# Optimization experiments

Measured on AMD Instinct MI355X. Metric: run time of the kernel, lower is better.

The kernel has to match this reference:

```python
import jax, jax.numpy as jnp
import numpy as np

WIN = 8          # window_size
DIM = 96         # embedding dim
HEADS = 3        # num_heads
N = WIN * WIN    # tokens per window
B_ = 8192        # total windows (2 images * 64*64 windows)
NUM_WIN = 4096   # windows per image (mask leading dim)


def _relative_position_index():
    # Same construction as the torch module (meshgrid default 'ij').
    ch = np.arange(WIN)
    coords = np.stack(np.meshgrid(ch, ch, indexing="ij"))          # [2, W, W]
    flat = coords.reshape(2, -1)                                     # [2, N]
    rel = flat[:, :, None] - flat[:, None, :]                        # [2, N, N]
    rel = rel.transpose(1, 2, 0).astype(np.int32)                    # [N, N, 2]
    rel[:, :, 0] += WIN - 1
    rel[:, :, 1] += WIN - 1
    rel[:, :, 0] *= 2 * WIN - 1
    return rel.sum(-1)                                               # [N, N] int32


def setup_inputs() -> dict:
    key = jax.random.key(0)
    ks = jax.random.split(key, 8)
    x = jax.random.normal(ks[0], (B_, N, DIM), dtype=jnp.float32)
    mask = jax.random.normal(ks[1], (NUM_WIN, N, N), dtype=jnp.float32)
    s = 0.02
    qkv_w = jax.random.normal(ks[2], (3 * DIM, DIM), dtype=jnp.float32) * s
    qkv_b = jax.random.normal(ks[3], (3 * DIM,), dtype=jnp.float32) * s
    proj_w = jax.random.normal(ks[4], (DIM, DIM), dtype=jnp.float32) * s
    proj_b = jax.random.normal(ks[5], (DIM,), dtype=jnp.float32) * s
    n_bias = (2 * WIN - 1) * (2 * WIN - 1)  # 225
    bias_table = jax.random.normal(ks[6], (n_bias, HEADS), dtype=jnp.float32) * s
    rel_idx = jnp.asarray(_relative_position_index())  # [N, N] int32
    return {"x": x, "mask": mask, "qkv_w": qkv_w, "qkv_b": qkv_b,
            "proj_w": proj_w, "proj_b": proj_b, "bias_table": bias_table,
            "rel_idx": rel_idx}


def reference(x, mask, qkv_w, qkv_b, proj_w, proj_b, bias_table, rel_idx):
    Bw, n, C = x.shape
    hd = C // HEADS
    scale = hd ** (-0.5)
    qkv = (x @ qkv_w.T + qkv_b).reshape(Bw, n, 3, HEADS, hd)
    qkv = jnp.transpose(qkv, (2, 0, 3, 1, 4))
    q, k, v = qkv[0], qkv[1], qkv[2]
    attn = jnp.einsum("bhqd,bhkd->bhqk", q * scale, k)              # [Bw, H, n, n]
    # relative position bias gather: [n, n, H] -> [H, n, n]
    bias = bias_table[rel_idx.reshape(-1)].reshape(n, n, HEADS)
    attn = attn + jnp.transpose(bias, (2, 0, 1))[None]
    # shift mask: broadcast over (batch, heads)
    nw = mask.shape[0]
    attn = attn.reshape(Bw // nw, nw, HEADS, n, n) + mask[None, :, None]
    attn = attn.reshape(Bw, HEADS, n, n)
    attn = jax.nn.softmax(attn, axis=-1)
    out = jnp.einsum("bhqk,bhkd->bhqd", attn, v)                    # [Bw, H, n, hd]
    out = jnp.transpose(out, (0, 2, 1, 3)).reshape(Bw, n, C)
    return out @ proj_w.T + proj_b
```

## Files before the change

### kernel.cpp

```cpp
#include <hip/hip_runtime.h>

typedef __attribute__((ext_vector_type(8))) short short8v;
typedef __attribute__((ext_vector_type(4))) float f32x4;

#define INVLN2 1.4426950408889634f

__device__ __forceinline__ ushort f2bf(float f) {
  union { float f; unsigned int u; } c; c.f = f;
  return (ushort)((c.u + 0x7FFFu + ((c.u >> 16) & 1u)) >> 16);
}

__device__ __forceinline__ unsigned cvtpk(float a, float b) {
  unsigned r;
  asm("v_cvt_pk_bf16_f32 %0, %1, %2" : "=v"(r) : "v"(a), "v"(b));
  return r;
}

__device__ __forceinline__ float exp2w(float x) {
#if __has_builtin(__builtin_amdgcn_exp2f)
  return __builtin_amdgcn_exp2f(x);
#else
  return __expf(x * 0.6931471805599453f);
#endif
}

__device__ __forceinline__ short8v bits8(unsigned a, unsigned b, unsigned c, unsigned d) {
  union { unsigned u[4]; short8v s; } cv;
  cv.u[0] = a; cv.u[1] = b; cv.u[2] = c; cv.u[3] = d;
  return cv.s;
}

__global__ __launch_bounds__(256) void setup_k(
    const float* __restrict__ qkv_w, const float* __restrict__ proj_w,
    const float* __restrict__ bias_table, const int* __restrict__ rel_idx,
    const float* __restrict__ qkv_b,
    ushort* __restrict__ qkv_wb, ushort* __restrict__ proj_wb,
    float* __restrict__ bias_comb, float* __restrict__ qkv_bs) {
  const float qs = 0.17677669529663687f * INVLN2;
  int idx = blockIdx.x * 256 + threadIdx.x;
  if (idx < 27648) {
    qkv_wb[idx] = f2bf(qkv_w[idx] * (idx < 9216 ? qs : 1.0f));
  } else if (idx < 36864) {
    int i = idx - 27648;
    int cw = i / 96, j = i % 96;
    int h = j >> 5, kk = j & 31;
    int g = kk >> 3, b = (kk & 4) >> 2, d = kk & 3;
    int src = h * 32 + 16 * b + 4 * g + d;
    proj_wb[i] = f2bf(proj_w[cw * 96 + src]);
  } else if (idx < 49152) {
    int i = idx - 36864;
    int h = i / 4096, rc = i % 4096;
    bias_comb[i] = bias_table[rel_idx[rc] * 3 + h] * INVLN2;
  } else if (idx < 49440) {
    int i = idx - 49152;
    qkv_bs[i] = qkv_b[i] * (i < 96 ? qs : 1.0f);
  }
}

__global__ __launch_bounds__(256, 2) void winattn(
    const float* __restrict__ x, const float* __restrict__ mask,
    const ushort* __restrict__ qkv_wb, const ushort* __restrict__ proj_wb,
    const float* __restrict__ bias_comb, const float* __restrict__ qkv_bs,
    const float* __restrict__ proj_b, float* __restrict__ out) {
  __shared__ ushort klds[2][64][104];
  __shared__ ushort vts[2][96][64];
  __shared__ ushort wq[29952];

  const int bb = blockIdx.x;
  const int t = threadIdx.x;
  const int w = t >> 6;
  const int lane = t & 63;
  const int l15 = lane & 15;
  const int g = lane >> 4;
  const int qrow = w * 16 + l15;

  float4 xr4[2][3][2];
  #pragma unroll
  for (int u = 0; u < 2; ++u) {
    const float* xr = x + ((size_t)(bb + u * 4096) * 64 + qrow) * 96 + g * 8;
    #pragma unroll
    for (int ks3 = 0; ks3 < 3; ++ks3) {
      xr4[u][ks3][0] = *reinterpret_cast<const float4*>(xr + ks3 * 32);
      xr4[u][ks3][1] = *reinterpret_cast<const float4*>(xr + ks3 * 32 + 4);
    }
  }
  const float* mrow = mask + (size_t)bb * 4096 + qrow * 64;
  float4 mk4[4];
  #pragma unroll
  for (int tj = 0; tj < 4; ++tj)
    mk4[tj] = *reinterpret_cast<const float4*>(mrow + tj * 16 + g * 4);

  #pragma unroll
  for (int i = 0; i < 14; ++i) {
    const int c = i * 256 + t;
    if (i < 13 || t < 128) {
      const int row = c / 12, cc = c % 12;
      short8v wv = *reinterpret_cast<const short8v*>(qkv_wb + row * 96 + cc * 8);
      *reinterpret_cast<short8v*>(&wq[row * 104 + cc * 8]) = wv;
    }
  }
  __syncthreads();

  short8v xa[2][3];
  #pragma unroll
  for (int u = 0; u < 2; ++u)
    #pragma unroll
    for (int ks3 = 0; ks3 < 3; ++ks3) {
      const float4 a0 = xr4[u][ks3][0], a1 = xr4[u][ks3][1];
      xa[u][ks3] = bits8(cvtpk(a0.x, a0.y), cvtpk(a0.z, a0.w),
                         cvtpk(a1.x, a1.y), cvtpk(a1.z, a1.w));
    }

  unsigned qpk[2][6][2];
  short8v bfA[3];
  float4 qbA = {0.f, 0.f, 0.f, 0.f}, qbB;
  float vbA = 0.f, vbB;
  {
    const ushort* wr = &wq[l15 * 104 + g * 8];
    bfA[0] = *reinterpret_cast<const short8v*>(wr);
    bfA[1] = *reinterpret_cast<const short8v*>(wr + 32);
    bfA[2] = *reinterpret_cast<const short8v*>(wr + 64);
    qbA = *reinterpret_cast<const float4*>(qkv_bs + g * 4);
  }
  #pragma unroll
  for (int nt = 0; nt < 18; ++nt) {
    short8v bfB[3];
    if (nt < 17) {
      const ushort* wr = &wq[((nt + 1) * 16 + l15) * 104 + g * 8];
      bfB[0] = *reinterpret_cast<const short8v*>(wr);
      bfB[1] = *reinterpret_cast<const short8v*>(wr + 32);
      bfB[2] = *reinterpret_cast<const short8v*>(wr + 64);
      if (nt + 1 < 12) qbB = *reinterpret_cast<const float4*>(qkv_bs + (nt + 1) * 16 + g * 4);
      else             vbB = qkv_bs[(nt + 1) * 16 + l15];
    }
    if (nt < 6) {
      #pragma unroll
      for (int u = 0; u < 2; ++u) {
        f32x4 acc = {0.f, 0.f, 0.f, 0.f};
        #pragma unroll
        for (int ks3 = 0; ks3 < 3; ++ks3)
          acc = __builtin_amdgcn_mfma_f32_16x16x32_bf16(bfA[ks3], xa[u][ks3], acc, 0, 0, 0);
        qpk[u][nt][0] = cvtpk(acc[0] + qbA.x, acc[1] + qbA.y);
        qpk[u][nt][1] = cvtpk(acc[2] + qbA.z, acc[3] + qbA.w);
      }
    } else if (nt < 12) {
      const int m = nt - 6;
      const int kcol = 32 * (m >> 1) + 8 * g + 4 * (m & 1);
      #pragma unroll
      for (int u = 0; u < 2; ++u) {
        f32x4 acc = {0.f, 0.f, 0.f, 0.f};
        #pragma unroll
        for (int ks3 = 0; ks3 < 3; ++ks3)
          acc = __builtin_amdgcn_mfma_f32_16x16x32_bf16(bfA[ks3], xa[u][ks3], acc, 0, 0, 0);
        uint2 pk = make_uint2(cvtpk(acc[0] + qbA.x, acc[1] + qbA.y),
                              cvtpk(acc[2] + qbA.z, acc[3] + qbA.w));
        *reinterpret_cast<uint2*>(&klds[u][qrow][kcol]) = pk;
      }
    } else {
      const int vc = nt * 16 + l15 - 192;
      const int tk = (32 * (w >> 1) + 8 * g + 4 * (w & 1)) ^ ((vc & 7) << 3);
      #pragma unroll
      for (int u = 0; u < 2; ++u) {
        f32x4 acc = {0.f, 0.f, 0.f, 0.f};
        #pragma unroll
        for (int ks3 = 0; ks3 < 3; ++ks3)
          acc = __builtin_amdgcn_mfma_f32_16x16x32_bf16(xa[u][ks3], bfA[ks3], acc, 0, 0, 0);
        uint2 pk = make_uint2(cvtpk(acc[0] + vbA, acc[1] + vbA),
                              cvtpk(acc[2] + vbA, acc[3] + vbA));
        *reinterpret_cast<uint2*>(&vts[u][vc][tk]) = pk;
      }
    }
    if (nt < 17) {
      bfA[0] = bfB[0]; bfA[1] = bfB[1]; bfA[2] = bfB[2];
      qbA = qbB; vbA = vbB;
    }
  }

  short8v qf[2][3];
  #pragma unroll
  for (int u = 0; u < 2; ++u)
    #pragma unroll
    for (int h = 0; h < 3; ++h)
      qf[u][h] = bits8(qpk[u][2 * h][0], qpk[u][2 * h][1],
                       qpk[u][2 * h + 1][0], qpk[u][2 * h + 1][1]);

  const float* bcb0 = bias_comb + qrow * 64;
  float bmk[3][4][4];
  #pragma unroll
  for (int h = 0; h < 3; ++h)
    #pragma unroll
    for (int tj = 0; tj < 4; ++tj) {
      float4 b4 = *reinterpret_cast<const float4*>(bcb0 + h * 4096 + tj * 16 + g * 4);
      bmk[h][tj][0] = b4.x + mk4[tj].x * INVLN2;
      bmk[h][tj][1] = b4.y + mk4[tj].y * INVLN2;
      bmk[h][tj][2] = b4.z + mk4[tj].z * INVLN2;
      bmk[h][tj][3] = b4.w + mk4[tj].w * INVLN2;
    }

  __syncthreads();

  short8v ofv[3][2];

  #pragma unroll
  for (int h = 0; h < 3; ++h) {
    f32x4 s[2][4];
    #pragma unroll
    for (int tj = 0; tj < 4; ++tj) {
      #pragma unroll
      for (int u = 0; u < 2; ++u) {
        short8v kf = *reinterpret_cast<const short8v*>(&klds[u][tj * 16 + l15][h * 32 + g * 8]);
        f32x4 z = {0.f, 0.f, 0.f, 0.f};
        s[u][tj] = __builtin_amdgcn_mfma_f32_16x16x32_bf16(kf, qf[u][h], z, 0, 0, 0);
      }
    }
    #pragma unroll
    for (int tj = 0; tj < 4; ++tj)
      #pragma unroll
      for (int u = 0; u < 2; ++u)
        #pragma unroll
        for (int r = 0; r < 4; ++r) s[u][tj][r] += bmk[h][tj][r];
    float inv[2];
    #pragma unroll
    for (int u = 0; u < 2; ++u) {
      #pragma unroll
      for (int tj = 0; tj < 4; ++tj)
        #pragma unroll
        for (int r = 0; r < 4; ++r) s[u][tj][r] = exp2w(s[u][tj][r]);
      float sm = ((s[u][0][0] + s[u][0][1]) + (s[u][0][2] + s[u][0][3]))
               + ((s[u][1][0] + s[u][1][1]) + (s[u][1][2] + s[u][1][3]))
               + ((s[u][2][0] + s[u][2][1]) + (s[u][2][2] + s[u][2][3]))
               + ((s[u][3][0] + s[u][3][1]) + (s[u][3][2] + s[u][3][3]));
      sm += __shfl_xor(sm, 16);
      sm += __shfl_xor(sm, 32);
      inv[u] = __builtin_amdgcn_rcpf(sm);
    }
    short8v pfv[2][2];
    #pragma unroll
    for (int u = 0; u < 2; ++u) {
      unsigned p00 = cvtpk(s[u][0][0], s[u][0][1]);
      unsigned p01 = cvtpk(s[u][0][2], s[u][0][3]);
      unsigned p10 = cvtpk(s[u][1][0], s[u][1][1]);
      unsigned p11 = cvtpk(s[u][1][2], s[u][1][3]);
      unsigned p20 = cvtpk(s[u][2][0], s[u][2][1]);
      unsigned p21 = cvtpk(s[u][2][2], s[u][2][3]);
      unsigned p30 = cvtpk(s[u][3][0], s[u][3][1]);
      unsigned p31 = cvtpk(s[u][3][2], s[u][3][3]);
      pfv[u][0] = bits8(p00, p01, p10, p11);
      pfv[u][1] = bits8(p20, p21, p30, p31);
    }
    #pragma unroll
    for (int u = 0; u < 2; ++u) {
      f32x4 oacc[2];
      #pragma unroll
      for (int nt = 0; nt < 2; ++nt) {
        const int vc = h * 32 + nt * 16 + l15;
        f32x4 o = {0.f, 0.f, 0.f, 0.f};
        #pragma unroll
        for (int ks2 = 0; ks2 < 2; ++ks2) {
          const int tk = (ks2 * 32 + g * 8) ^ ((vc & 7) << 3);
          short8v vf = *reinterpret_cast<const short8v*>(&vts[u][vc][tk]);
          o = __builtin_amdgcn_mfma_f32_16x16x32_bf16(vf, pfv[u][ks2], o, 0, 0, 0);
        }
        oacc[nt] = o;
      }
      unsigned o00 = cvtpk(oacc[0][0] * inv[u], oacc[0][1] * inv[u]);
      unsigned o01 = cvtpk(oacc[0][2] * inv[u], oacc[0][3] * inv[u]);
      unsigned o10 = cvtpk(oacc[1][0] * inv[u], oacc[1][1] * inv[u]);
      unsigned o11 = cvtpk(oacc[1][2] * inv[u], oacc[1][3] * inv[u]);
      ofv[h][u] = bits8(o00, o01, o10, o11);
    }
  }

  f32x4 pacc[2][6];
  #pragma unroll
  for (int u = 0; u < 2; ++u)
    #pragma unroll
    for (int nt2 = 0; nt2 < 6; ++nt2) pacc[u][nt2] = (f32x4){0.f, 0.f, 0.f, 0.f};
  #pragma unroll
  for (int h = 0; h < 3; ++h) {
    #pragma unroll
    for (int nt2 = 0; nt2 < 6; ++nt2) {
      short8v pfw = *reinterpret_cast<const short8v*>(proj_wb + (nt2 * 16 + l15) * 96 + h * 32 + g * 8);
      #pragma unroll
      for (int u = 0; u < 2; ++u)
        pacc[u][nt2] = __builtin_amdgcn_mfma_f32_16x16x32_bf16(ofv[h][u], pfw, pacc[u][nt2], 0, 0, 0);
    }
  }

  float pb[6];
  #pragma unroll
  for (int nt2 = 0; nt2 < 6; ++nt2) pb[nt2] = proj_b[nt2 * 16 + l15];
  #pragma unroll
  for (int u = 0; u < 2; ++u) {
    float* ob = out + (size_t)(bb + u * 4096) * 6144 + (w * 16 + g * 4) * 96 + l15;
    #pragma unroll
    for (int nt2 = 0; nt2 < 6; ++nt2)
      #pragma unroll
      for (int r = 0; r < 4; ++r)
        ob[r * 96 + nt2 * 16] = pacc[u][nt2][r] + pb[nt2];
  }
}

extern "C" void kernel_launch(void* const* d_in, const int* in_sizes, int n_in,
                              void* d_out, int out_size, void* d_ws, size_t ws_size,
                              hipStream_t stream) {
  const float* x          = (const float*)d_in[0];
  const float* mask       = (const float*)d_in[1];
  const float* qkv_w      = (const float*)d_in[2];
  const float* qkv_b      = (const float*)d_in[3];
  const float* proj_w     = (const float*)d_in[4];
  const float* proj_b     = (const float*)d_in[5];
  const float* bias_table = (const float*)d_in[6];
  const int*   rel_idx    = (const int*)d_in[7];

  char* ws = (char*)d_ws;
  ushort* qkv_wb    = (ushort*)ws;
  ushort* proj_wb   = (ushort*)(ws + 55296);
  float*  bias_comb = (float*)(ws + 55296 + 18432);
  float*  qkv_bs    = (float*)(ws + 55296 + 18432 + 49152);

  setup_k<<<194, 256, 0, stream>>>(qkv_w, proj_w, bias_table, rel_idx, qkv_b,
                                   qkv_wb, proj_wb, bias_comb, qkv_bs);
  winattn<<<4096, 256, 0, stream>>>(x, mask, qkv_wb, proj_wb,
                                    bias_comb, qkv_bs, proj_b, (float*)d_out);
}
```

Before: 182.6 us.

## Process four windows per 512-thread block to amortize weight staging

Doubles the block to 512 threads, split into two groups of four waves, and gives each group two windows, so one block handles four windows and the grid halves to 2048 blocks. The 56KB QKV weight copy into shared memory is now shared across four windows instead of two, which cuts the global-to-LDS staging traffic and the per-block setup. In exchange, shared-memory use per block rises (K and V buffers double), which may limit how many blocks fit per CU, and each block is larger and coarser to schedule.

After: 152.9 us. -16.3%, faster.

```diff
diff --git a/kernel.cpp b/kernel.cpp
--- a/kernel.cpp
+++ b/kernel.cpp
@@ -57,43 +57,48 @@
   }
 }
 
-__global__ __launch_bounds__(256, 2) void winattn(
+__global__ __launch_bounds__(512, 2) void winattn(
     const float* __restrict__ x, const float* __restrict__ mask,
     const ushort* __restrict__ qkv_wb, const ushort* __restrict__ proj_wb,
     const float* __restrict__ bias_comb, const float* __restrict__ qkv_bs,
     const float* __restrict__ proj_b, float* __restrict__ out) {
-  __shared__ ushort klds[2][64][104];
-  __shared__ ushort vts[2][96][64];
+  __shared__ ushort klds[4][64][104];
+  __shared__ ushort vts[4][96][64];
   __shared__ ushort wq[29952];
 
   const int bb = blockIdx.x;
   const int t = threadIdx.x;
   const int w = t >> 6;
+  const int grp = w >> 2;
+  const int wl = w & 3;
   const int lane = t & 63;
   const int l15 = lane & 15;
   const int g = lane >> 4;
-  const int qrow = w * 16 + l15;
+  const int qrow = wl * 16 + l15;
+
 
   float4 xr4[2][3][2];
   #pragma unroll
-  for (int u = 0; u < 2; ++u) {
-    const float* xr = x + ((size_t)(bb + u * 4096) * 64 + qrow) * 96 + g * 8;
+  for (int uu = 0; uu < 2; ++uu) {
+    const int u = grp * 2 + uu;
+    const int win = bb + ((u >> 1) << 11) + ((u & 1) << 12);
+    const float* xr = x + ((size_t)win * 64 + qrow) * 96 + g * 8;
     #pragma unroll
     for (int ks3 = 0; ks3 < 3; ++ks3) {
-      xr4[u][ks3][0] = *reinterpret_cast<const float4*>(xr + ks3 * 32);
-      xr4[u][ks3][1] = *reinterpret_cast<const float4*>(xr + ks3 * 32 + 4);
-    }
-  }
-  const float* mrow = mask + (size_t)bb * 4096 + qrow * 64;
+      xr4[uu][ks3][0] = *reinterpret_cast<const float4*>(xr + ks3 * 32);
+      xr4[uu][ks3][1] = *reinterpret_cast<const float4*>(xr + ks3 * 32 + 4);
+    }
+  }
+  const float* mrow = mask + (size_t)(bb + (grp << 11)) * 4096 + qrow * 64;
   float4 mk4[4];
   #pragma unroll
   for (int tj = 0; tj < 4; ++tj)
     mk4[tj] = *reinterpret_cast<const float4*>(mrow + tj * 16 + g * 4);
 
   #pragma unroll
-  for (int i = 0; i < 14; ++i) {
-    const int c = i * 256 + t;
-    if (i < 13 || t < 128) {
+  for (int i = 0; i < 7; ++i) {
+    const int c = i * 512 + t;
+    if (i < 6 || t < 384) {
       const int row = c / 12, cc = c % 12;
       short8v wv = *reinterpret_cast<const short8v*>(qkv_wb + row * 96 + cc * 8);
       *reinterpret_cast<short8v*>(&wq[row * 104 + cc * 8]) = wv;
@@ -103,12 +108,12 @@
 
   short8v xa[2][3];
   #pragma unroll
-  for (int u = 0; u < 2; ++u)
+  for (int uu = 0; uu < 2; ++uu)
     #pragma unroll
     for (int ks3 = 0; ks3 < 3; ++ks3) {
-      const float4 a0 = xr4[u][ks3][0], a1 = xr4[u][ks3][1];
-      xa[u][ks3] = bits8(cvtpk(a0.x, a0.y), cvtpk(a0.z, a0.w),
-                         cvtpk(a1.x, a1.y), cvtpk(a1.z, a1.w));
+      const float4 a0 = xr4[uu][ks3][0], a1 = xr4[uu][ks3][1];
+      xa[uu][ks3] = bits8(cvtpk(a0.x, a0.y), cvtpk(a0.z, a0.w),
+                          cvtpk(a1.x, a1.y), cvtpk(a1.z, a1.w));
     }
 
   unsigned qpk[2][6][2];
@@ -135,36 +140,38 @@
     }
     if (nt < 6) {
       #pragma unroll
-      for (int u = 0; u < 2; ++u) {
+      for (int uu = 0; uu < 2; ++uu) {
         f32x4 acc = {0.f, 0.f, 0.f, 0.f};
         #pragma unroll
         for (int ks3 = 0; ks3 < 3; ++ks3)
-          acc = __builtin_amdgcn_mfma_f32_16x16x32_bf16(bfA[ks3], xa[u][ks3], acc, 0, 0, 0);
-        qpk[u][nt][0] = cvtpk(acc[0] + qbA.x, acc[1] + qbA.y);
-        qpk[u][nt][1] = cvtpk(acc[2] + qbA.z, acc[3] + qbA.w);
+          acc = __builtin_amdgcn_mfma_f32_16x16x32_bf16(bfA[ks3], xa[uu][ks3], acc, 0, 0, 0);
+        qpk[uu][nt][0] = cvtpk(acc[0] + qbA.x, acc[1] + qbA.y);
+        qpk[uu][nt][1] = cvtpk(acc[2] + qbA.z, acc[3] + qbA.w);
       }
     } else if (nt < 12) {
       const int m = nt - 6;
       const int kcol = 32 * (m >> 1) + 8 * g + 4 * (m & 1);
       #pragma unroll
-      for (int u = 0; u < 2; ++u) {
+      for (int uu = 0; uu < 2; ++uu) {
+        const int u = grp * 2 + uu;
         f32x4 acc = {0.f, 0.f, 0.f, 0.f};
         #pragma unroll
         for (int ks3 = 0; ks3 < 3; ++ks3)
-          acc = __builtin_amdgcn_mfma_f32_16x16x32_bf16(bfA[ks3], xa[u][ks3], acc, 0, 0, 0);
+          acc = __builtin_amdgcn_mfma_f32_16x16x32_bf16(bfA[ks3], xa[uu][ks3], acc, 0, 0, 0);
         uint2 pk = make_uint2(cvtpk(acc[0] + qbA.x, acc[1] + qbA.y),
                               cvtpk(acc[2] + qbA.z, acc[3] + qbA.w));
         *reinterpret_cast<uint2*>(&klds[u][qrow][kcol]) = pk;
       }
     } else {
       const int vc = nt * 16 + l15 - 192;
-      const int tk = (32 * (w >> 1) + 8 * g + 4 * (w & 1)) ^ ((vc & 7) << 3);
-      #pragma unroll
-      for (int u = 0; u < 2; ++u) {
+      const int tk = (32 * (wl >> 1) + 8 * g + 4 * (wl & 1)) ^ ((vc & 7) << 3);
+      #pragma unroll
+      for (int uu = 0; uu < 2; ++uu) {
+        const int u = grp * 2 + uu;
         f32x4 acc = {0.f, 0.f, 0.f, 0.f};
         #pragma unroll
         for (int ks3 = 0; ks3 < 3; ++ks3)
-          acc = __builtin_amdgcn_mfma_f32_16x16x32_bf16(xa[u][ks3], bfA[ks3], acc, 0, 0, 0);
+          acc = __builtin_amdgcn_mfma_f32_16x16x32_bf16(xa[uu][ks3], bfA[ks3], acc, 0, 0, 0);
         uint2 pk = make_uint2(cvtpk(acc[0] + vbA, acc[1] + vbA),
                               cvtpk(acc[2] + vbA, acc[3] + vbA));
         *reinterpret_cast<uint2*>(&vts[u][vc][tk]) = pk;
@@ -178,11 +185,11 @@
 
   short8v qf[2][3];
   #pragma unroll
-  for (int u = 0; u < 2; ++u)
+  for (int uu = 0; uu < 2; ++uu)
     #pragma unroll
     for (int h = 0; h < 3; ++h)
-      qf[u][h] = bits8(qpk[u][2 * h][0], qpk[u][2 * h][1],
-                       qpk[u][2 * h + 1][0], qpk[u][2 * h + 1][1]);
+      qf[uu][h] = bits8(qpk[uu][2 * h][0], qpk[uu][2 * h][1],
+                        qpk[uu][2 * h + 1][0], qpk[uu][2 * h + 1][1]);
 
   const float* bcb0 = bias_comb + qrow * 64;
   float bmk[3][4][4];
@@ -207,49 +214,51 @@
     #pragma unroll
     for (int tj = 0; tj < 4; ++tj) {
       #pragma unroll
-      for (int u = 0; u < 2; ++u) {
+      for (int uu = 0; uu < 2; ++uu) {
+        const int u = grp * 2 + uu;
         short8v kf = *reinterpret_cast<const short8v*>(&klds[u][tj * 16 + l15][h * 32 + g * 8]);
         f32x4 z = {0.f, 0.f, 0.f, 0.f};
-        s[u][tj] = __builtin_amdgcn_mfma_f32_16x16x32_bf16(kf, qf[u][h], z, 0, 0, 0);
+        s[uu][tj] = __builtin_amdgcn_mfma_f32_16x16x32_bf16(kf, qf[uu][h], z, 0, 0, 0);
       }
     }
     #pragma unroll
     for (int tj = 0; tj < 4; ++tj)
       #pragma unroll
-      for (int u = 0; u < 2; ++u)
-        #pragma unroll
-        for (int r = 0; r < 4; ++r) s[u][tj][r] += bmk[h][tj][r];
+      for (int uu = 0; uu < 2; ++uu)
+        #pragma unroll
+        for (int r = 0; r < 4; ++r) s[uu][tj][r] += bmk[h][tj][r];
     float inv[2];
     #pragma unroll
-    for (int u = 0; u < 2; ++u) {
+    for (int uu = 0; uu < 2; ++uu) {
       #pragma unroll
       for (int tj = 0; tj < 4; ++tj)
         #pragma unroll
-        for (int r = 0; r < 4; ++r) s[u][tj][r] = exp2w(s[u][tj][r]);
-      float sm = ((s[u][0][0] + s[u][0][1]) + (s[u][0][2] + s[u][0][3]))
-               + ((s[u][1][0] + s[u][1][1]) + (s[u][1][2] + s[u][1][3]))
-               + ((s[u][2][0] + s[u][2][1]) + (s[u][2][2] + s[u][2][3]))
-               + ((s[u][3][0] + s[u][3][1]) + (s[u][3][2] + s[u][3][3]));
+        for (int r = 0; r < 4; ++r) s[uu][tj][r] = exp2w(s[uu][tj][r]);
+      float sm = ((s[uu][0][0] + s[uu][0][1]) + (s[uu][0][2] + s[uu][0][3]))
+               + ((s[uu][1][0] + s[uu][1][1]) + (s[uu][1][2] + s[uu][1][3]))
+               + ((s[uu][2][0] + s[uu][2][1]) + (s[uu][2][2] + s[uu][2][3]))
+               + ((s[uu][3][0] + s[uu][3][1]) + (s[uu][3][2] + s[uu][3][3]));
       sm += __shfl_xor(sm, 16);
       sm += __shfl_xor(sm, 32);
-      inv[u] = __builtin_amdgcn_rcpf(sm);
+      inv[uu] = __builtin_amdgcn_rcpf(sm);
     }
     short8v pfv[2][2];
     #pragma unroll
-    for (int u = 0; u < 2; ++u) {
-      unsigned p00 = cvtpk(s[u][0][0], s[u][0][1]);
-      unsigned p01 = cvtpk(s[u][0][2], s[u][0][3]);
-      unsigned p10 = cvtpk(s[u][1][0], s[u][1][1]);
-      unsigned p11 = cvtpk(s[u][1][2], s[u][1][3]);
-      unsigned p20 = cvtpk(s[u][2][0], s[u][2][1]);
-      unsigned p21 = cvtpk(s[u][2][2], s[u][2][3]);
-      unsigned p30 = cvtpk(s[u][3][0], s[u][3][1]);
-      unsigned p31 = cvtpk(s[u][3][2], s[u][3][3]);
-      pfv[u][0] = bits8(p00, p01, p10, p11);
-      pfv[u][1] = bits8(p20, p21, p30, p31);
-    }
-    #pragma unroll
-    for (int u = 0; u < 2; ++u) {
+    for (int uu = 0; uu < 2; ++uu) {
+      unsigned p00 = cvtpk(s[uu][0][0], s[uu][0][1]);
+      unsigned p01 = cvtpk(s[uu][0][2], s[uu][0][3]);
+      unsigned p10 = cvtpk(s[uu][1][0], s[uu][1][1]);
+      unsigned p11 = cvtpk(s[uu][1][2], s[uu][1][3]);
+      unsigned p20 = cvtpk(s[uu][2][0], s[uu][2][1]);
+      unsigned p21 = cvtpk(s[uu][2][2], s[uu][2][3]);
+      unsigned p30 = cvtpk(s[uu][3][0], s[uu][3][1]);
+      unsigned p31 = cvtpk(s[uu][3][2], s[uu][3][3]);
+      pfv[uu][0] = bits8(p00, p01, p10, p11);
+      pfv[uu][1] = bits8(p20, p21, p30, p31);
+    }
+    #pragma unroll
+    for (int uu = 0; uu < 2; ++uu) {
+      const int u = grp * 2 + uu;
       f32x4 oacc[2];
       #pragma unroll
       for (int nt = 0; nt < 2; ++nt) {
@@ -259,31 +268,31 @@
         for (int ks2 = 0; ks2 < 2; ++ks2) {
           const int tk = (ks2 * 32 + g * 8) ^ ((vc & 7) << 3);
           short8v vf = *reinterpret_cast<const short8v*>(&vts[u][vc][tk]);
-          o = __builtin_amdgcn_mfma_f32_16x16x32_bf16(vf, pfv[u][ks2], o, 0, 0, 0);
+          o = __builtin_amdgcn_mfma_f32_16x16x32_bf16(vf, pfv[uu][ks2], o, 0, 0, 0);
         }
         oacc[nt] = o;
       }
-      unsigned o00 = cvtpk(oacc[0][0] * inv[u], oacc[0][1] * inv[u]);
-      unsigned o01 = cvtpk(oacc[0][2] * inv[u], oacc[0][3] * inv[u]);
-      unsigned o10 = cvtpk(oacc[1][0] * inv[u], oacc[1][1] * inv[u]);
-      unsigned o11 = cvtpk(oacc[1][2] * inv[u], oacc[1][3] * inv[u]);
-      ofv[h][u] = bits8(o00, o01, o10, o11);
+      unsigned o00 = cvtpk(oacc[0][0] * inv[uu], oacc[0][1] * inv[uu]);
+      unsigned o01 = cvtpk(oacc[0][2] * inv[uu], oacc[0][3] * inv[uu]);
+      unsigned o10 = cvtpk(oacc[1][0] * inv[uu], oacc[1][1] * inv[uu]);
+      unsigned o11 = cvtpk(oacc[1][2] * inv[uu], oacc[1][3] * inv[uu]);
+      ofv[h][uu] = bits8(o00, o01, o10, o11);
     }
   }
 
   f32x4 pacc[2][6];
   #pragma unroll
-  for (int u = 0; u < 2; ++u)
-    #pragma unroll
-    for (int nt2 = 0; nt2 < 6; ++nt2) pacc[u][nt2] = (f32x4){0.f, 0.f, 0.f, 0.f};
+  for (int uu = 0; uu < 2; ++uu)
+    #pragma unroll
+    for (int nt2 = 0; nt2 < 6; ++nt2) pacc[uu][nt2] = (f32x4){0.f, 0.f, 0.f, 0.f};
   #pragma unroll
   for (int h = 0; h < 3; ++h) {
     #pragma unroll
     for (int nt2 = 0; nt2 < 6; ++nt2) {
       short8v pfw = *reinterpret_cast<const short8v*>(proj_wb + (nt2 * 16 + l15) * 96 + h * 32 + g * 8);
       #pragma unroll
-      for (int u = 0; u < 2; ++u)
-        pacc[u][nt2] = __builtin_amdgcn_mfma_f32_16x16x32_bf16(ofv[h][u], pfw, pacc[u][nt2], 0, 0, 0);
+      for (int uu = 0; uu < 2; ++uu)
+        pacc[uu][nt2] = __builtin_amdgcn_mfma_f32_16x16x32_bf16(ofv[h][uu], pfw, pacc[uu][nt2], 0, 0, 0);
     }
   }
 
@@ -291,13 +300,15 @@
   #pragma unroll
   for (int nt2 = 0; nt2 < 6; ++nt2) pb[nt2] = proj_b[nt2 * 16 + l15];
   #pragma unroll
-  for (int u = 0; u < 2; ++u) {
-    float* ob = out + (size_t)(bb + u * 4096) * 6144 + (w * 16 + g * 4) * 96 + l15;
+  for (int uu = 0; uu < 2; ++uu) {
+    const int u = grp * 2 + uu;
+    const int win = bb + ((u >> 1) << 11) + ((u & 1) << 12);
+    float* ob = out + (size_t)win * 6144 + (wl * 16 + g * 4) * 96 + l15;
     #pragma unroll
     for (int nt2 = 0; nt2 < 6; ++nt2)
       #pragma unroll
       for (int r = 0; r < 4; ++r)
-        ob[r * 96 + nt2 * 16] = pacc[u][nt2][r] + pb[nt2];
+        ob[r * 96 + nt2 * 16] = pacc[uu][nt2][r] + pb[nt2];
   }
 }
 
@@ -321,6 +332,6 @@
 
   setup_k<<<194, 256, 0, stream>>>(qkv_w, proj_w, bias_table, rel_idx, qkv_b,
                                    qkv_wb, proj_wb, bias_comb, qkv_bs);
-  winattn<<<4096, 256, 0, stream>>>(x, mask, qkv_wb, proj_wb,
+  winattn<<<2048, 512, 0, stream>>>(x, mask, qkv_wb, proj_wb,
                                     bias_comb, qkv_bs, proj_b, (float*)d_out);
 }
```
